# Kernel tuning notes

Hardware: AMD Instinct MI355X
Metric: run time of the kernel (lower is better)

Reference implementation:

```python
import jax, jax.numpy as jnp
import numpy as np
import math

N = 50000          # nodes
E = 1000000        # edges (avg degree 20)
NGRAPH = 64        # graphs in batch
CIN = 16           # input scalar channels (16x0e)
C = 32             # hidden multiplicity (mul)
OUT = 100          # output scalars per graph (100x0e)
NB = 10            # number_of_basis
MAX_RADIUS = 3.5
NUM_NEIGH = 20.0
NUM_NODES = 781.25 # 50000 / 64


def setup_inputs() -> dict:
    key = jax.random.key(0)
    ks = jax.random.split(key, 24)
    def p(k, shape, fan):
        return jax.random.normal(k, shape, jnp.float32) / math.sqrt(fan)
    inp = {}
    inp['pos'] = jax.random.normal(ks[0], (N, 3), jnp.float32)
    inp['x'] = jax.random.normal(ks[1], (N, CIN), jnp.float32)
    inp['z'] = jnp.ones((N, 1), jnp.float32)
    inp['edge_index'] = jax.random.randint(ks[2], (2, E), 0, N)
    inp['edge_shift'] = jnp.zeros((E, 3), jnp.float32)
    inp['lattice'] = jax.random.normal(ks[3], (NGRAPH, 3, 3), jnp.float32) * 0.01
    inp['batch'] = jnp.sort(jax.random.randint(ks[4], (N,), 0, NGRAPH))
    inp['fc1_w0'] = p(ks[5], (NB, 100), NB)
    inp['fc1_w1'] = p(ks[6], (100, 2 * CIN), 100)
    inp['sc1'] = p(ks[7], (CIN, 2 * C), CIN)
    inp['lin1_s'] = p(ks[8], (CIN, 2 * C), CIN)
    inp['lin1_v'] = p(ks[9], (CIN, C), CIN)
    inp['fc2_w0'] = p(ks[10], (NB, 100), NB)
    inp['fc2_w1'] = p(ks[11], (100, 5 * C), 100)
    inp['sc2_s'] = p(ks[12], (C, 2 * C), C)
    inp['sc2_v'] = p(ks[13], (C, C), C)
    inp['lin2_s'] = p(ks[14], (C, 2 * C), C)
    inp['lin2_v'] = p(ks[15], (C, C), C)
    inp['fco_w0'] = p(ks[16], (NB, 100), NB)
    inp['fco_w1'] = p(ks[17], (100, 2 * C), 100)
    inp['sco'] = p(ks[18], (C, OUT), C)
    inp['lino_s'] = p(ks[19], (C, OUT), C)
    return inp


def _edge_features(pos, edge_index, edge_shift, lattice, batch):
    src, dst = edge_index[0], edge_index[1]
    ebatch = batch[src]
    # preprocess: edge vectors with periodic shift correction
    edge_vec = pos[dst] - pos[src] + jnp.einsum('ni,nij->nj', edge_shift, lattice[ebatch])
    r = jnp.linalg.norm(edge_vec, axis=1)
    rhat = edge_vec / jnp.maximum(r, 1e-12)[:, None]
    # spherical harmonics lmax=1, component normalization: Y0 = 1, Y1 = sqrt(3) * rhat
    sh0 = jnp.ones_like(r)
    sh1 = math.sqrt(3.0) * rhat
    # soft_one_hot_linspace, basis='gaussian', cutoff=False, scaled by sqrt(NB)
    values = jnp.linspace(0.0, MAX_RADIUS, NB)
    step = values[1] - values[0]
    diff = (r[:, None] - values[None, :]) / step
    basis = jnp.exp(-diff * diff) / 1.12 * math.sqrt(NB)
    # smooth_cutoff(r / max_radius)
    u = 2.0 * (r / MAX_RADIUS - 1.0)
    cut = jnp.where(u > 0, 0.0, jnp.where(u < -2.0, 1.0, 0.5 * (1.0 - jnp.cos(math.pi * u))))
    return src, dst, cut * sh0, cut[:, None] * sh1, basis


def _seg(m, dst):
    return jax.ops.segment_sum(m, dst, num_segments=N) / math.sqrt(NUM_NEIGH)


def reference(pos, x, z, edge_index, edge_shift, lattice, batch,
              fc1_w0, fc1_w1, sc1, lin1_s, lin1_v,
              fc2_w0, fc2_w1, sc2_s, sc2_v, lin2_s, lin2_v,
              fco_w0, fco_w1, sco, lino_s):
    src, dst, sh0, sh1, basis = _edge_features(pos, edge_index, edge_shift, lattice, batch)

    # ---- layer 1: 16x0e input -> gated (C x 0e, C x 1o) ----
    w = jax.nn.silu(basis @ fc1_w0) @ fc1_w1           # (E, 2*CIN) radial weights
    s_src = x[src]                                     # (E, CIN)
    m_s = w[:, :CIN] * s_src * sh0[:, None]            # 0e x Y0 -> 0e
    m_v = (w[:, CIN:] * s_src)[:, :, None] * sh1[:, None, :]  # 0e x Y1 -> 1o
    a_s = _seg(m_s, dst)                               # (N, CIN)
    a_v = _seg(m_v, dst)                               # (N, CIN, 3)
    s_h = (x * z) @ sc1 + a_s @ lin1_s                 # (N, 2C) scalars+gates
    v_h = jnp.einsum('nci,co->noi', a_v, lin1_v)       # (N, C, 3)
    s = jax.nn.silu(s_h[:, :C])
    v = v_h * jax.nn.sigmoid(s_h[:, C:])[:, :, None]

    # ---- layer 2: (C x 0e, C x 1o) -> gated (C x 0e, C x 1o) ----
    w = jax.nn.silu(basis @ fc2_w0) @ fc2_w1           # (E, 5C)
    w1, w2, w3, w4, w5 = jnp.split(w, 5, axis=1)
    ss = s[src]                                        # (E, C)
    vs = v[src]                                        # (E, C, 3)
    m_s = w1 * ss * sh0[:, None] + w2 * jnp.einsum('eci,ei->ec', vs, sh1)
    m_v = (w3 * ss)[:, :, None] * sh1[:, None, :] \
        + w4[:, :, None] * vs * sh0[:, None, None] \
        + w5[:, :, None] * jnp.cross(vs, sh1[:, None, :])
    a_s = _seg(m_s, dst)
    a_v = _seg(m_v, dst)
    s_h = (s * z) @ sc2_s + a_s @ lin2_s
    v_h = jnp.einsum('nci,co->noi', v, sc2_v) + jnp.einsum('nci,co->noi', a_v, lin2_v)
    s2 = jax.nn.silu(s_h[:, :C])
    v2 = v_h * jax.nn.sigmoid(s_h[:, C:])[:, :, None]

    # ---- output convolution: -> 100x0e per node ----
    w = jax.nn.silu(basis @ fco_w0) @ fco_w1           # (E, 2C)
    w1, w2 = jnp.split(w, 2, axis=1)
    m = w1 * s2[src] * sh0[:, None] + w2 * jnp.einsum('eci,ei->ec', v2[src], sh1)
    a = _seg(m, dst)                                   # (N, C)
    out_nodes = (s2 * z) @ sco + a @ lino_s            # (N, OUT)

    # reduce_output: scatter over graphs, divide sqrt(num_nodes)
    out = jax.ops.segment_sum(out_nodes, batch, num_segments=NGRAPH) / math.sqrt(NUM_NODES)
    return out
```

## Files before the change

### kernel.cpp

```cpp
#include <hip/hip_runtime.h>
#include <hip/hip_bf16.h>

#define NN 50000
#define EE 1000000
#define NGRAPHS 64
#define NB_N 196
#define NB_E 3907
#define NB_X 3125
#define NB_T 1563
#define NTAB 4096
#define SPL 16

#define INV_SQRT_NEIGH 0.22360679774997896f
#define INV_SQRT_NODES 0.035777087639996634f
#define SQRT3 1.7320508075688772f
#define BSCALE 2.8234621879136734f
#define BSTEP 0.3888888888888889f
#define INV_BSTEP 2.5714285714285716f
#define PI_F 3.14159265358979323846f
#define TAB_DR (3.5f / 4095.0f)
#define TAB_SCALE (4095.0f / 3.5f)

__device__ __forceinline__ float silu_f(float x) { return x / (1.0f + __expf(-x)); }
__device__ __forceinline__ float sigm_f(float x) { return 1.0f / (1.0f + __expf(-x)); }

__device__ __forceinline__ unsigned short f2bf(float f) {
    union { float f; unsigned u; } v; v.f = f;
    unsigned r = v.u + 0x7fffu + ((v.u >> 16) & 1u);
    return (unsigned short)(r >> 16);
}
__device__ __forceinline__ unsigned pk2(float a, float b) {
    return (unsigned)f2bf(a) | ((unsigned)f2bf(b) << 16);
}
__device__ __forceinline__ float bflo(unsigned u) { return __uint_as_float(u << 16); }
__device__ __forceinline__ float bfhi(unsigned u) { return __uint_as_float(u & 0xffff0000u); }

__global__ __launch_bounds__(256) void k_tab(
    const float* __restrict__ fc1w0, const float* __restrict__ fc1w1,
    const float* __restrict__ fc2w0, const float* __restrict__ fc2w1,
    const float* __restrict__ fcow0, const float* __restrict__ fcow1,
    float* __restrict__ tab1, unsigned short* __restrict__ tab2b,
    unsigned short* __restrict__ tab3b)
{
    __shared__ float h[3][100];
    int entry = blockIdx.x;
    int t = threadIdx.x;
    float r = entry * TAB_DR;
    float b[10];
#pragma unroll
    for (int i = 0; i < 10; ++i) {
        float d = (r - (float)i * BSTEP) * INV_BSTEP;
        b[i] = __expf(-d * d) * BSCALE;
    }
    for (int job = t; job < 300; job += 256) {
        int tb = job / 100;
        int j = job - tb * 100;
        const float* w0 = (tb == 0) ? fc1w0 : (tb == 1 ? fc2w0 : fcow0);
        float a = 0.0f;
#pragma unroll
        for (int i = 0; i < 10; ++i) a += b[i] * w0[i * 100 + j];
        h[tb][j] = silu_f(a);
    }
    __syncthreads();
    if (t < 32) {
        float acc = 0.0f;
        for (int j = 0; j < 100; ++j) acc += h[0][j] * fc1w1[j * 32 + t];
        tab1[(size_t)entry * 32 + t] = acc;
    } else if (t < 192) {
        int o = t - 32;
        float acc = 0.0f;
        for (int j = 0; j < 100; ++j) acc += h[1][j] * fc2w1[j * 160 + o];
        tab2b[((size_t)entry * 32 + (o & 31)) * 8 + (o >> 5)] = f2bf(acc);
    } else {
        int o = t - 192;
        float acc = 0.0f;
        for (int j = 0; j < 100; ++j) acc += h[2][j] * fcow1[j * 64 + o];
        tab3b[((size_t)entry * 32 + (o & 31)) * 2 + (o >> 5)] = f2bf(acc);
    }
}

__global__ __launch_bounds__(256) void k_pre2(
    const int* __restrict__ batch, int* __restrict__ gstart,
    const int* __restrict__ ei, int* __restrict__ deg,
    const float* __restrict__ x, unsigned short* __restrict__ row0)
{
    int blk = blockIdx.x;
    if (blk < NB_N) {
        int n = blk * 256 + threadIdx.x;
        if (n >= NN) return;
        int b = batch[n];
        if (n == 0) { for (int g = 0; g <= b; ++g) gstart[g] = 0; }
        else {
            int pb = batch[n - 1];
            for (int g = pb + 1; g <= b; ++g) gstart[g] = n;
        }
        if (n == NN - 1) { for (int g = b + 1; g <= NGRAPHS; ++g) gstart[g] = NN; }
    } else if (blk < NB_N + NB_E) {
        int e = (blk - NB_N) * 256 + threadIdx.x;
        if (e < EE) atomicAdd(&deg[ei[EE + e]], 1);
    } else {
        int idx = (blk - NB_N - NB_E) * 256 + threadIdx.x;
        if (idx < NN * 16) row0[idx] = f2bf(x[idx]);
    }
}

__global__ __launch_bounds__(256) void k_scan1(const int* __restrict__ deg, int* __restrict__ bsum)
{
    __shared__ int sd[256];
    int t = threadIdx.x;
    int i = blockIdx.x * 256 + t;
    sd[t] = (i < NN) ? deg[i] : 0;
    __syncthreads();
#pragma unroll
    for (int o = 128; o > 0; o >>= 1) {
        if (t < o) sd[t] += sd[t + o];
        __syncthreads();
    }
    if (t == 0) bsum[blockIdx.x] = sd[0];
}

__global__ void k_scan2(const int* __restrict__ bsum, int* __restrict__ boff, int* __restrict__ rowp)
{
    if (threadIdx.x == 0) {
        int acc = 0;
        for (int b = 0; b < NB_N; ++b) { boff[b] = acc; acc += bsum[b]; }
        rowp[NN] = EE;
    }
}

__global__ __launch_bounds__(256) void k_scan3(
    const int* __restrict__ deg, const int* __restrict__ boff,
    int* __restrict__ rowp, int* __restrict__ cursor)
{
    __shared__ int sd[256];
    int t = threadIdx.x;
    int i = blockIdx.x * 256 + t;
    int v = (i < NN) ? deg[i] : 0;
    sd[t] = v;
    __syncthreads();
#pragma unroll
    for (int o = 1; o < 256; o <<= 1) {
        int xv = 0;
        if (t >= o) xv = sd[t - o];
        __syncthreads();
        sd[t] += xv;
        __syncthreads();
    }
    if (i < NN) {
        int val = boff[blockIdx.x] + sd[t] - v;
        rowp[i] = val;
        cursor[i] = val;
    }
}

__global__ __launch_bounds__(256) void k_geom(
    const float* __restrict__ pos, const int* __restrict__ ei,
    const float* __restrict__ eshift, const float* __restrict__ lat,
    const int* __restrict__ batch, int* __restrict__ cursor,
    uint4* __restrict__ rec)
{
    int e = blockIdx.x * 256 + threadIdx.x;
    if (e >= EE) return;
    int src = ei[e];
    int dst = ei[EE + e];
    int g = batch[src];
    const float* L = lat + g * 9;
    float t0 = eshift[e*3+0], t1 = eshift[e*3+1], t2 = eshift[e*3+2];
    float vx = pos[dst*3+0] - pos[src*3+0] + t0*L[0] + t1*L[3] + t2*L[6];
    float vy = pos[dst*3+1] - pos[src*3+1] + t0*L[1] + t1*L[4] + t2*L[7];
    float vz = pos[dst*3+2] - pos[src*3+2] + t0*L[2] + t1*L[5] + t2*L[8];
    float r = sqrtf(vx*vx + vy*vy + vz*vz);
    float u = 2.0f * (r * (1.0f/3.5f) - 1.0f);
    float cut;
    if (u > 0.0f) cut = 0.0f;
    else if (u < -2.0f) cut = 1.0f;
    else cut = 0.5f * (1.0f - __cosf(PI_F * u));
    float inv = 1.0f / fmaxf(r, 1e-12f);
    float sc = SQRT3 * cut * inv;
    int i0 = (int)fminf(r * TAB_SCALE + 0.5f, 4095.0f);
    int slot = atomicAdd(&cursor[dst], 1);
    rec[slot] = make_uint4(pk2(sc * vx, sc * vy), pk2(sc * vz, 0.0f),
                           (unsigned)src | ((unsigned)i0 << 17),
                           __float_as_uint(cut));
}

#define EREC_DECODE(E)                                  \
    float cs_ = __uint_as_float((E).w);                 \
    float cx_ = bflo((E).x);                            \
    float cy_ = bfhi((E).x);                            \
    float cz_ = bflo((E).y);                            \
    int src_ = (int)((E).z & 0x1ffffu);                 \
    int i0_ = (int)((E).z >> 17);

#define F1_EDGE(E, ACC) {                                           \
    EREC_DECODE(E)                                                  \
    float w_ = tab1[(size_t)i0_ * 32 + toff];                       \
    float xs_ = __uint_as_float((unsigned)row0[src_ * 16 + c] << 16); \
    float gs_ = (q == 0) ? cs_ : (q == 1 ? cx_ : (q == 2 ? cy_ : cz_)); \
    ACC += w_ * xs_ * gs_; }

__global__ __launch_bounds__(256) void k_fuse1(
    const int* __restrict__ rowp, const uint4* __restrict__ rec,
    const float* __restrict__ tab1, const unsigned short* __restrict__ row0,
    float* __restrict__ a1)
{
    int wid = (blockIdx.x * 256 + threadIdx.x) >> 6;
    int l = threadIdx.x & 63;
    if (wid >= NN) return;
    int b0 = __builtin_amdgcn_readfirstlane(rowp[wid]);
    int b1 = __builtin_amdgcn_readfirstlane(rowp[wid + 1]);
    int q = l >> 4, c = l & 15;
    int toff = (q ? 16 : 0) + c;
    float aA = 0.0f, aB = 0.0f, aC = 0.0f, aD = 0.0f;
    int s = b0;
    for (; s + 3 < b1; s += 4) {
        uint4 eA = rec[s], eB = rec[s+1], eC = rec[s+2], eD = rec[s+3];
        F1_EDGE(eA, aA) F1_EDGE(eB, aB) F1_EDGE(eC, aC) F1_EDGE(eD, aD)
    }
    for (; s < b1; ++s) {
        uint4 eA = rec[s];
        F1_EDGE(eA, aA)
    }
    a1[(size_t)wid * 64 + l] = (aA + aB) + (aC + aD);
}

#define F2_EDGE(E, AS, AX, AY, AZ) {                                \
    EREC_DECODE(E)                                                  \
    uint4 tv_ = ((const uint4*)tab2b)[(size_t)i0_ * 32 + c];        \
    uint2 rv_ = ((const uint2*)row1)[(size_t)src_ * 32 + c];        \
    float w1_ = bflo(tv_.x), w2_ = bfhi(tv_.x);                     \
    float w3_ = bflo(tv_.y), w4_ = bfhi(tv_.y);                     \
    float w5_ = bflo(tv_.z);                                        \
    float sv_ = bflo(rv_.x), vx_ = bfhi(rv_.x);                     \
    float vy_ = bflo(rv_.y), vz_ = bfhi(rv_.y);                     \
    float dot_ = vx_ * cx_ + vy_ * cy_ + vz_ * cz_;                 \
    float w3s_ = w3_ * sv_, w4c_ = w4_ * cs_;                       \
    AS += w1_ * sv_ * cs_ + w2_ * dot_;                             \
    AX += w3s_ * cx_ + w4c_ * vx_ + w5_ * (vy_ * cz_ - vz_ * cy_);  \
    AY += w3s_ * cy_ + w4c_ * vy_ + w5_ * (vz_ * cx_ - vx_ * cz_);  \
    AZ += w3s_ * cz_ + w4c_ * vz_ + w5_ * (vx_ * cy_ - vy_ * cx_); }

__global__ __launch_bounds__(256) void k_fuse2(
    const int* __restrict__ rowp, const uint4* __restrict__ rec,
    const unsigned short* __restrict__ tab2b, const unsigned short* __restrict__ row1,
    float* __restrict__ a2)
{
    int wid = (blockIdx.x * 256 + threadIdx.x) >> 6;
    int l = threadIdx.x & 63;
    if (wid >= NN) return;
    int b0 = __builtin_amdgcn_readfirstlane(rowp[wid]);
    int b1 = __builtin_amdgcn_readfirstlane(rowp[wid + 1]);
    int p = l >> 5, c = l & 31;
    float s0 = 0, x0 = 0, y0 = 0, z0 = 0;
    float s1a = 0, x1 = 0, y1 = 0, z1 = 0;
    int s = b0 + p;
    for (; s + 4 < b1; s += 6) {
        uint4 eA = rec[s], eB = rec[s+2], eC = rec[s+4];
        F2_EDGE(eA, s0, x0, y0, z0)
        F2_EDGE(eB, s1a, x1, y1, z1)
        F2_EDGE(eC, s0, x0, y0, z0)
    }
    for (; s < b1; s += 2) {
        uint4 eA = rec[s];
        F2_EDGE(eA, s1a, x1, y1, z1)
    }
    float mS = s0 + s1a, mX = x0 + x1, mY = y0 + y1, mZ = z0 + z1;
    mS += __shfl_xor(mS, 32);
    mX += __shfl_xor(mX, 32);
    mY += __shfl_xor(mY, 32);
    mZ += __shfl_xor(mZ, 32);
    if (p == 0) {
        float* ap = a2 + (size_t)wid * 128;
        ap[c]      = mS;
        ap[32 + c] = mX;
        ap[64 + c] = mY;
        ap[96 + c] = mZ;
    }
}

#define F3_EDGE(E, ACC) {                                           \
    EREC_DECODE(E)                                                  \
    unsigned tv_ = ((const unsigned*)tab3b)[(size_t)i0_ * 32 + c];  \
    uint2 rv_ = ((const uint2*)row2)[(size_t)src_ * 32 + c];        \
    float w1_ = bflo(tv_), w2_ = bfhi(tv_);                         \
    float sv_ = bflo(rv_.x), vx_ = bfhi(rv_.x);                     \
    float vy_ = bflo(rv_.y), vz_ = bfhi(rv_.y);                     \
    float dot_ = vx_ * cx_ + vy_ * cy_ + vz_ * cz_;                 \
    ACC += w1_ * sv_ * cs_ + w2_ * dot_; }

__global__ __launch_bounds__(256) void k_fuse3(
    const int* __restrict__ rowp, const uint4* __restrict__ rec,
    const unsigned short* __restrict__ tab3b, const unsigned short* __restrict__ row2,
    float* __restrict__ a3)
{
    int wid = (blockIdx.x * 256 + threadIdx.x) >> 6;
    int l = threadIdx.x & 63;
    if (wid >= NN) return;
    int b0 = __builtin_amdgcn_readfirstlane(rowp[wid]);
    int b1 = __builtin_amdgcn_readfirstlane(rowp[wid + 1]);
    int p = l >> 5, c = l & 31;
    float aA = 0.0f, aB = 0.0f;
    int s = b0 + p;
    for (; s + 6 < b1; s += 8) {
        uint4 eA = rec[s], eB = rec[s+2], eC = rec[s+4], eD = rec[s+6];
        F3_EDGE(eA, aA) F3_EDGE(eB, aB) F3_EDGE(eC, aA) F3_EDGE(eD, aB)
    }
    for (; s < b1; s += 2) {
        uint4 eA = rec[s];
        F3_EDGE(eA, aA)
    }
    float acc = aA + aB;
    acc += __shfl_xor(acc, 32);
    if (p == 0) a3[(size_t)wid * 32 + c] = acc;
}

__global__ __launch_bounds__(256) void k_node1(
    const float* __restrict__ x, const float* __restrict__ z,
    const float* __restrict__ a1,
    const float* __restrict__ sc1, const float* __restrict__ lin1s,
    const float* __restrict__ lin1v,
    ushort4* __restrict__ row1)
{
    __shared__ float xz[32][20];
    __shared__ float am[32][68];
    __shared__ float shb[32][68];
    int t = threadIdx.x;
    int base = blockIdx.x * 32;
    if (t < 128) {
        int node = t >> 2, rem = t & 3;
        if (base + node < NN)
            *(float4*)&xz[node][rem * 4] = ((const float4*)x)[(size_t)(base + node) * 4 + rem];
    }
#pragma unroll
    for (int k = 0; k < 2; ++k) {
        int f = k * 256 + t;
        int node = f >> 4, rem = f & 15;
        if (base + node < NN)
            *(float4*)&am[node][rem * 4] = ((const float4*)a1)[(size_t)(base + node) * 16 + rem];
    }
    __syncthreads();
    int node = t >> 3, og = t & 7;
    int gnode = base + node;
    float zz = (gnode < NN) ? z[gnode] : 0.0f;
    int o0 = og * 8;
    float acc[8];
#pragma unroll
    for (int k = 0; k < 8; ++k) acc[k] = 0.0f;
#pragma unroll
    for (int c = 0; c < 16; ++c) {
        float xc = xz[node][c] * zz;
        float ac = am[node][c] * INV_SQRT_NEIGH;
        float4 wa = *(const float4*)&sc1[c * 64 + o0];
        float4 wb = *(const float4*)&sc1[c * 64 + o0 + 4];
        float4 la = *(const float4*)&lin1s[c * 64 + o0];
        float4 lb = *(const float4*)&lin1s[c * 64 + o0 + 4];
        acc[0] += xc * wa.x + ac * la.x;
        acc[1] += xc * wa.y + ac * la.y;
        acc[2] += xc * wa.z + ac * la.z;
        acc[3] += xc * wa.w + ac * la.w;
        acc[4] += xc * wb.x + ac * lb.x;
        acc[5] += xc * wb.y + ac * lb.y;
        acc[6] += xc * wb.z + ac * lb.z;
        acc[7] += xc * wb.w + ac * lb.w;
    }
#pragma unroll
    for (int k = 0; k < 8; ++k) shb[node][o0 + k] = acc[k];
    __syncthreads();
    int o0v = og * 4;
    float a4[3][4];
#pragma unroll
    for (int i = 0; i < 3; ++i)
#pragma unroll
        for (int k = 0; k < 4; ++k) a4[i][k] = 0.0f;
#pragma unroll
    for (int c = 0; c < 16; ++c) {
        float4 lv = *(const float4*)&lin1v[c * 32 + o0v];
#pragma unroll
        for (int i = 0; i < 3; ++i) {
            float av = am[node][16 + i * 16 + c] * INV_SQRT_NEIGH;
            a4[i][0] += av * lv.x; a4[i][1] += av * lv.y;
            a4[i][2] += av * lv.z; a4[i][3] += av * lv.w;
        }
    }
    if (gnode < NN) {
#pragma unroll
        for (int k = 0; k < 4; ++k) {
            float so = silu_f(shb[node][o0v + k]);
            float gt = sigm_f(shb[node][32 + o0v + k]);
            row1[(size_t)gnode * 32 + o0v + k] =
                make_ushort4(f2bf(so), f2bf(a4[0][k] * gt), f2bf(a4[1][k] * gt), f2bf(a4[2][k] * gt));
        }
    }
}

__global__ __launch_bounds__(256) void k_node2(
    const float* __restrict__ z,
    const uint2* __restrict__ row1, const float* __restrict__ a2,
    const float* __restrict__ sc2s, const float* __restrict__ sc2v,
    const float* __restrict__ lin2s, const float* __restrict__ lin2v,
    float* __restrict__ s2, ushort4* __restrict__ row2)
{
    __shared__ uint2 rw[32][33];
    __shared__ float am[32][132];
    __shared__ float shb[32][68];
    int t = threadIdx.x;
    int base = blockIdx.x * 32;
    {
        int node = t >> 3, rem = t & 7;
        if (base + node < NN) {
            const uint2* rp = row1 + (size_t)(base + node) * 32;
#pragma unroll
            for (int k = 0; k < 4; ++k)
                rw[node][rem * 4 + k] = rp[rem * 4 + k];
        }
    }
#pragma unroll
    for (int k = 0; k < 4; ++k) {
        int f = k * 256 + t;
        int node = f >> 5, rem = f & 31;
        if (base + node < NN)
            *(float4*)&am[node][rem * 4] = ((const float4*)a2)[(size_t)(base + node) * 32 + rem];
    }
    __syncthreads();
    int node = t >> 3, og = t & 7;
    int gnode = base + node;
    float zz = (gnode < NN) ? z[gnode] : 0.0f;
    int o0 = og * 8;
    float acc[8];
#pragma unroll
    for (int k = 0; k < 8; ++k) acc[k] = 0.0f;
#pragma unroll 8
    for (int c = 0; c < 32; ++c) {
        float sv = bflo(rw[node][c].x) * zz;
        float ac = am[node][c] * INV_SQRT_NEIGH;
        float4 wa = *(const float4*)&sc2s[c * 64 + o0];
        float4 wb = *(const float4*)&sc2s[c * 64 + o0 + 4];
        float4 la = *(const float4*)&lin2s[c * 64 + o0];
        float4 lb = *(const float4*)&lin2s[c * 64 + o0 + 4];
        acc[0] += sv * wa.x + ac * la.x;
        acc[1] += sv * wa.y + ac * la.y;
        acc[2] += sv * wa.z + ac * la.z;
        acc[3] += sv * wa.w + ac * la.w;
        acc[4] += sv * wb.x + ac * lb.x;
        acc[5] += sv * wb.y + ac * lb.y;
        acc[6] += sv * wb.z + ac * lb.z;
        acc[7] += sv * wb.w + ac * lb.w;
    }
#pragma unroll
    for (int k = 0; k < 8; ++k) shb[node][o0 + k] = acc[k];
    __syncthreads();
    int o0v = og * 4;
    float a4[3][4];
#pragma unroll
    for (int i = 0; i < 3; ++i)
#pragma unroll
        for (int k = 0; k < 4; ++k) a4[i][k] = 0.0f;
#pragma unroll 8
    for (int c = 0; c < 32; ++c) {
        float4 wv = *(const float4*)&sc2v[c * 32 + o0v];
        float4 lv = *(const float4*)&lin2v[c * 32 + o0v];
        uint2 rv = rw[node][c];
        float vvv[3];
        vvv[0] = bfhi(rv.x); vvv[1] = bflo(rv.y); vvv[2] = bfhi(rv.y);
#pragma unroll
        for (int i = 0; i < 3; ++i) {
            float av = am[node][32 + i * 32 + c] * INV_SQRT_NEIGH;
            a4[i][0] += vvv[i] * wv.x + av * lv.x;
            a4[i][1] += vvv[i] * wv.y + av * lv.y;
            a4[i][2] += vvv[i] * wv.z + av * lv.z;
            a4[i][3] += vvv[i] * wv.w + av * lv.w;
        }
    }
    if (gnode < NN) {
#pragma unroll
        for (int k = 0; k < 4; ++k) {
            float so = silu_f(shb[node][o0v + k]);
            float gt = sigm_f(shb[node][32 + o0v + k]);
            s2[gnode * 32 + o0v + k] = so;
            row2[(size_t)gnode * 32 + o0v + k] =
                make_ushort4(f2bf(so), f2bf(a4[0][k] * gt), f2bf(a4[1][k] * gt), f2bf(a4[2][k] * gt));
        }
    }
}

__global__ __launch_bounds__(256) void k_red(
    const float* __restrict__ z, const int* __restrict__ gstart,
    const float* __restrict__ s2, const float* __restrict__ a3,
    float* __restrict__ pbuf)
{
    int g  = blockIdx.x >> 4;
    int sp = blockIdx.x & (SPL - 1);
    int n0 = gstart[g], n1 = gstart[g + 1];
    int per = (n1 - n0 + SPL - 1) / SPL;
    int a = n0 + sp * per;
    int b = a + per; if (b > n1) b = n1;
    int t = threadIdx.x;
    int comp = t & 63;
    int lane = t >> 6;
    float acc = 0.0f;
    for (int n = a + lane; n < b; n += 4) {
        if (comp < 32) acc += s2[n * 32 + comp] * z[n];
        else           acc += a3[(size_t)n * 32 + (comp - 32)];
    }
    __shared__ float sd[256];
    sd[t] = acc;
    __syncthreads();
    if (t < 64)
        pbuf[(size_t)blockIdx.x * 64 + t] = sd[t] + sd[t + 64] + sd[t + 128] + sd[t + 192];
}

__global__ __launch_bounds__(128) void k_out2(
    const float* __restrict__ pbuf, const float* __restrict__ sco,
    const float* __restrict__ lino, float* __restrict__ out)
{
    __shared__ float A[32], B[32];
    int g = blockIdx.x;
    int t = threadIdx.x;
    if (t < 64) {
        float v = 0.0f;
        for (int sp = 0; sp < SPL; ++sp)
            v += pbuf[(size_t)(g * SPL + sp) * 64 + t];
        if (t < 32) A[t] = v;
        else        B[t - 32] = v * INV_SQRT_NEIGH;
    }
    __syncthreads();
    if (t < 100) {
        float res = 0.0f;
#pragma unroll
        for (int c = 0; c < 32; ++c)
            res += A[c] * sco[c * 100 + t] + B[c] * lino[c * 100 + t];
        out[g * 100 + t] = res * INV_SQRT_NODES;
    }
}

extern "C" void kernel_launch(void* const* d_in, const int* in_sizes, int n_in,
                              void* d_out, int out_size, void* d_ws, size_t ws_size,
                              hipStream_t stream)
{
    const float* pos   = (const float*)d_in[0];
    const float* x     = (const float*)d_in[1];
    const float* z     = (const float*)d_in[2];
    const int*   ei    = (const int*)d_in[3];
    const float* esh   = (const float*)d_in[4];
    const float* lat   = (const float*)d_in[5];
    const int*   batch = (const int*)d_in[6];
    const float* fc1w0 = (const float*)d_in[7];
    const float* fc1w1 = (const float*)d_in[8];
    const float* sc1   = (const float*)d_in[9];
    const float* lin1s = (const float*)d_in[10];
    const float* lin1v = (const float*)d_in[11];
    const float* fc2w0 = (const float*)d_in[12];
    const float* fc2w1 = (const float*)d_in[13];
    const float* sc2s  = (const float*)d_in[14];
    const float* sc2v  = (const float*)d_in[15];
    const float* lin2s = (const float*)d_in[16];
    const float* lin2v = (const float*)d_in[17];
    const float* fcow0 = (const float*)d_in[18];
    const float* fcow1 = (const float*)d_in[19];
    const float* sco   = (const float*)d_in[20];
    const float* lino  = (const float*)d_in[21];
    float* out = (float*)d_out;

    char* cur = (char*)d_ws;
    auto alloc = [&](size_t bytes) { char* r = cur; cur += (bytes + 15) & ~(size_t)15; return r; };

    float* a1    = (float*)alloc((size_t)NN * 64 * 4);
    float* a2    = (float*)alloc((size_t)NN * 128 * 4);
    float* a3    = (float*)alloc((size_t)NN * 32 * 4);
    float* s2    = (float*)alloc((size_t)NN * 32 * 4);
    unsigned short* row0 = (unsigned short*)alloc((size_t)NN * 16 * 2);
    ushort4* row1 = (ushort4*)alloc((size_t)NN * 32 * 8);
    ushort4* row2 = (ushort4*)alloc((size_t)NN * 32 * 8);
    float* tab1  = (float*)alloc((size_t)NTAB * 32 * 4);
    unsigned short* tab2b = (unsigned short*)alloc((size_t)NTAB * 32 * 8 * 2);
    unsigned short* tab3b = (unsigned short*)alloc((size_t)NTAB * 32 * 2 * 2);
    float* pbuf  = (float*)alloc((size_t)NGRAPHS * SPL * 64 * 4);
    int* deg     = (int*)alloc((size_t)NN * 4);
    int* rowp    = (int*)alloc((size_t)(NN + 4) * 4);
    int* cursor  = (int*)alloc((size_t)NN * 4);
    int* bsum    = (int*)alloc(256 * 4);
    int* boff    = (int*)alloc(256 * 4);
    int* gstart  = (int*)alloc(68 * 4);
    uint4* rec   = (uint4*)alloc((size_t)EE * 16);

    (void)hipMemsetAsync(deg, 0, (size_t)NN * 4, stream);

    k_tab<<<NTAB, 256, 0, stream>>>(fc1w0, fc1w1, fc2w0, fc2w1, fcow0, fcow1,
                                    tab1, tab2b, tab3b);
    k_pre2<<<NB_N + NB_E + NB_X, 256, 0, stream>>>(batch, gstart, ei, deg, x, row0);

    k_scan1<<<NB_N, 256, 0, stream>>>(deg, bsum);
    k_scan2<<<1, 64, 0, stream>>>(bsum, boff, rowp);
    k_scan3<<<NB_N, 256, 0, stream>>>(deg, boff, rowp, cursor);
    k_geom <<<NB_E, 256, 0, stream>>>(pos, ei, esh, lat, batch, cursor, rec);

    int fb = (NN * 64 + 255) / 256;
    k_fuse1<<<fb, 256, 0, stream>>>(rowp, rec, tab1, row0, a1);
    k_node1<<<NB_T, 256, 0, stream>>>(x, z, a1, sc1, lin1s, lin1v, row1);
    k_fuse2<<<fb, 256, 0, stream>>>(rowp, rec, tab2b, (const unsigned short*)row1, a2);
    k_node2<<<NB_T, 256, 0, stream>>>(z, (const uint2*)row1, a2, sc2s, sc2v, lin2s, lin2v, s2, row2);
    k_fuse3<<<fb, 256, 0, stream>>>(rowp, rec, tab3b, (const unsigned short*)row2, a3);
    k_red<<<NGRAPHS * SPL, 256, 0, stream>>>(z, gstart, s2, a3, pbuf);
    k_out2<<<NGRAPHS, 128, 0, stream>>>(pbuf, sco, lino, out);
}
```

Measured before the change: 368.6 us.

## Merge table and preprocessing kernels, store conv2 table as fp32, unroll fuse2

Folds the radial-table kernel into the preprocessing kernel so a single launch covers table build, graph starts, degree counting and bf16 conversion. The conv2 weight table is now stored in fp32 rather than bf16, removing the unpacking work and bf16 rounding at the cost of twice the table footprint (4 MB). The fuse2 edge loop is unrolled from three to four edges per step. The table is indexed by the gathered edge radius, so the wider fp32 entries may put more pressure on the cache.

```diff
diff --git a/kernel.cpp b/kernel.cpp
--- a/kernel.cpp
+++ b/kernel.cpp
@@ -35,58 +35,55 @@
 __device__ __forceinline__ float bflo(unsigned u) { return __uint_as_float(u << 16); }
 __device__ __forceinline__ float bfhi(unsigned u) { return __uint_as_float(u & 0xffff0000u); }
 
-__global__ __launch_bounds__(256) void k_tab(
+__global__ __launch_bounds__(256) void k_pre3(
     const float* __restrict__ fc1w0, const float* __restrict__ fc1w1,
     const float* __restrict__ fc2w0, const float* __restrict__ fc2w1,
     const float* __restrict__ fcow0, const float* __restrict__ fcow1,
-    float* __restrict__ tab1, unsigned short* __restrict__ tab2b,
-    unsigned short* __restrict__ tab3b)
-{
-    __shared__ float h[3][100];
-    int entry = blockIdx.x;
-    int t = threadIdx.x;
-    float r = entry * TAB_DR;
-    float b[10];
-#pragma unroll
-    for (int i = 0; i < 10; ++i) {
-        float d = (r - (float)i * BSTEP) * INV_BSTEP;
-        b[i] = __expf(-d * d) * BSCALE;
-    }
-    for (int job = t; job < 300; job += 256) {
-        int tb = job / 100;
-        int j = job - tb * 100;
-        const float* w0 = (tb == 0) ? fc1w0 : (tb == 1 ? fc2w0 : fcow0);
-        float a = 0.0f;
-#pragma unroll
-        for (int i = 0; i < 10; ++i) a += b[i] * w0[i * 100 + j];
-        h[tb][j] = silu_f(a);
-    }
-    __syncthreads();
-    if (t < 32) {
-        float acc = 0.0f;
-        for (int j = 0; j < 100; ++j) acc += h[0][j] * fc1w1[j * 32 + t];
-        tab1[(size_t)entry * 32 + t] = acc;
-    } else if (t < 192) {
-        int o = t - 32;
-        float acc = 0.0f;
-        for (int j = 0; j < 100; ++j) acc += h[1][j] * fc2w1[j * 160 + o];
-        tab2b[((size_t)entry * 32 + (o & 31)) * 8 + (o >> 5)] = f2bf(acc);
-    } else {
-        int o = t - 192;
-        float acc = 0.0f;
-        for (int j = 0; j < 100; ++j) acc += h[2][j] * fcow1[j * 64 + o];
-        tab3b[((size_t)entry * 32 + (o & 31)) * 2 + (o >> 5)] = f2bf(acc);
-    }
-}
-
-__global__ __launch_bounds__(256) void k_pre2(
+    float* __restrict__ tab1, float* __restrict__ tab2f,
+    unsigned short* __restrict__ tab3b,
     const int* __restrict__ batch, int* __restrict__ gstart,
     const int* __restrict__ ei, int* __restrict__ deg,
     const float* __restrict__ x, unsigned short* __restrict__ row0)
 {
     int blk = blockIdx.x;
-    if (blk < NB_N) {
-        int n = blk * 256 + threadIdx.x;
+    int t = threadIdx.x;
+    if (blk < NTAB) {
+        __shared__ float h[3][100];
+        int entry = blk;
+        float r = entry * TAB_DR;
+        float b[10];
+#pragma unroll
+        for (int i = 0; i < 10; ++i) {
+            float d = (r - (float)i * BSTEP) * INV_BSTEP;
+            b[i] = __expf(-d * d) * BSCALE;
+        }
+        for (int job = t; job < 300; job += 256) {
+            int tb = job / 100;
+            int j = job - tb * 100;
+            const float* w0 = (tb == 0) ? fc1w0 : (tb == 1 ? fc2w0 : fcow0);
+            float a = 0.0f;
+#pragma unroll
+            for (int i = 0; i < 10; ++i) a += b[i] * w0[i * 100 + j];
+            h[tb][j] = silu_f(a);
+        }
+        __syncthreads();
+        if (t < 32) {
+            float acc = 0.0f;
+            for (int j = 0; j < 100; ++j) acc += h[0][j] * fc1w1[j * 32 + t];
+            tab1[(size_t)entry * 32 + t] = acc;
+        } else if (t < 192) {
+            int o = t - 32;
+            float acc = 0.0f;
+            for (int j = 0; j < 100; ++j) acc += h[1][j] * fc2w1[j * 160 + o];
+            tab2f[((size_t)entry * 32 + (o & 31)) * 8 + (o >> 5)] = acc;
+        } else {
+            int o = t - 192;
+            float acc = 0.0f;
+            for (int j = 0; j < 100; ++j) acc += h[2][j] * fcow1[j * 64 + o];
+            tab3b[((size_t)entry * 32 + (o & 31)) * 2 + (o >> 5)] = f2bf(acc);
+        }
+    } else if (blk < NTAB + NB_N) {
+        int n = (blk - NTAB) * 256 + t;
         if (n >= NN) return;
         int b = batch[n];
         if (n == 0) { for (int g = 0; g <= b; ++g) gstart[g] = 0; }
@@ -95,11 +92,11 @@
             for (int g = pb + 1; g <= b; ++g) gstart[g] = n;
         }
         if (n == NN - 1) { for (int g = b + 1; g <= NGRAPHS; ++g) gstart[g] = NN; }
-    } else if (blk < NB_N + NB_E) {
-        int e = (blk - NB_N) * 256 + threadIdx.x;
+    } else if (blk < NTAB + NB_N + NB_E) {
+        int e = (blk - NTAB - NB_N) * 256 + t;
         if (e < EE) atomicAdd(&deg[ei[EE + e]], 1);
     } else {
-        int idx = (blk - NB_N - NB_E) * 256 + threadIdx.x;
+        int idx = (blk - NTAB - NB_N - NB_E) * 256 + t;
         if (idx < NN * 16) row0[idx] = f2bf(x[idx]);
     }
 }
@@ -226,23 +223,22 @@
 
 #define F2_EDGE(E, AS, AX, AY, AZ) {                                \
     EREC_DECODE(E)                                                  \
-    uint4 tv_ = ((const uint4*)tab2b)[(size_t)i0_ * 32 + c];        \
+    const float* tp_ = tab2f + ((size_t)i0_ * 32 + c) * 8;          \
+    float4 w14_ = *(const float4*)tp_;                              \
+    float w5_ = tp_[4];                                             \
     uint2 rv_ = ((const uint2*)row1)[(size_t)src_ * 32 + c];        \
-    float w1_ = bflo(tv_.x), w2_ = bfhi(tv_.x);                     \
-    float w3_ = bflo(tv_.y), w4_ = bfhi(tv_.y);                     \
-    float w5_ = bflo(tv_.z);                                        \
     float sv_ = bflo(rv_.x), vx_ = bfhi(rv_.x);                     \
     float vy_ = bflo(rv_.y), vz_ = bfhi(rv_.y);                     \
     float dot_ = vx_ * cx_ + vy_ * cy_ + vz_ * cz_;                 \
-    float w3s_ = w3_ * sv_, w4c_ = w4_ * cs_;                       \
-    AS += w1_ * sv_ * cs_ + w2_ * dot_;                             \
+    float w3s_ = w14_.z * sv_, w4c_ = w14_.w * cs_;                 \
+    AS += w14_.x * sv_ * cs_ + w14_.y * dot_;                       \
     AX += w3s_ * cx_ + w4c_ * vx_ + w5_ * (vy_ * cz_ - vz_ * cy_);  \
     AY += w3s_ * cy_ + w4c_ * vy_ + w5_ * (vz_ * cx_ - vx_ * cz_);  \
     AZ += w3s_ * cz_ + w4c_ * vz_ + w5_ * (vx_ * cy_ - vy_ * cx_); }
 
 __global__ __launch_bounds__(256) void k_fuse2(
     const int* __restrict__ rowp, const uint4* __restrict__ rec,
-    const unsigned short* __restrict__ tab2b, const unsigned short* __restrict__ row1,
+    const float* __restrict__ tab2f, const unsigned short* __restrict__ row1,
     float* __restrict__ a2)
 {
     int wid = (blockIdx.x * 256 + threadIdx.x) >> 6;
@@ -254,11 +250,12 @@
     float s0 = 0, x0 = 0, y0 = 0, z0 = 0;
     float s1a = 0, x1 = 0, y1 = 0, z1 = 0;
     int s = b0 + p;
-    for (; s + 4 < b1; s += 6) {
-        uint4 eA = rec[s], eB = rec[s+2], eC = rec[s+4];
+    for (; s + 6 < b1; s += 8) {
+        uint4 eA = rec[s], eB = rec[s+2], eC = rec[s+4], eD = rec[s+6];
         F2_EDGE(eA, s0, x0, y0, z0)
         F2_EDGE(eB, s1a, x1, y1, z1)
         F2_EDGE(eC, s0, x0, y0, z0)
+        F2_EDGE(eD, s1a, x1, y1, z1)
     }
     for (; s < b1; s += 2) {
         uint4 eA = rec[s];
@@ -572,7 +569,7 @@
     ushort4* row1 = (ushort4*)alloc((size_t)NN * 32 * 8);
     ushort4* row2 = (ushort4*)alloc((size_t)NN * 32 * 8);
     float* tab1  = (float*)alloc((size_t)NTAB * 32 * 4);
-    unsigned short* tab2b = (unsigned short*)alloc((size_t)NTAB * 32 * 8 * 2);
+    float* tab2f = (float*)alloc((size_t)NTAB * 32 * 8 * 4);
     unsigned short* tab3b = (unsigned short*)alloc((size_t)NTAB * 32 * 2 * 2);
     float* pbuf  = (float*)alloc((size_t)NGRAPHS * SPL * 64 * 4);
     int* deg     = (int*)alloc((size_t)NN * 4);
@@ -585,9 +582,9 @@
 
     (void)hipMemsetAsync(deg, 0, (size_t)NN * 4, stream);
 
-    k_tab<<<NTAB, 256, 0, stream>>>(fc1w0, fc1w1, fc2w0, fc2w1, fcow0, fcow1,
-                                    tab1, tab2b, tab3b);
-    k_pre2<<<NB_N + NB_E + NB_X, 256, 0, stream>>>(batch, gstart, ei, deg, x, row0);
+    k_pre3<<<NTAB + NB_N + NB_E + NB_X, 256, 0, stream>>>(
+        fc1w0, fc1w1, fc2w0, fc2w1, fcow0, fcow1, tab1, tab2f, tab3b,
+        batch, gstart, ei, deg, x, row0);
 
     k_scan1<<<NB_N, 256, 0, stream>>>(deg, bsum);
     k_scan2<<<1, 64, 0, stream>>>(bsum, boff, rowp);
@@ -597,7 +594,7 @@
     int fb = (NN * 64 + 255) / 256;
     k_fuse1<<<fb, 256, 0, stream>>>(rowp, rec, tab1, row0, a1);
     k_node1<<<NB_T, 256, 0, stream>>>(x, z, a1, sc1, lin1s, lin1v, row1);
-    k_fuse2<<<fb, 256, 0, stream>>>(rowp, rec, tab2b, (const unsigned short*)row1, a2);
+    k_fuse2<<<fb, 256, 0, stream>>>(rowp, rec, tab2f, (const unsigned short*)row1, a2);
     k_node2<<<NB_T, 256, 0, stream>>>(z, (const uint2*)row1, a2, sc2s, sc2v, lin2s, lin2v, s2, row2);
     k_fuse3<<<fb, 256, 0, stream>>>(rowp, rec, tab3b, (const unsigned short*)row2, a3);
     k_red<<<NGRAPHS * SPL, 256, 0, stream>>>(z, gstart, s2, a3, pbuf);
```

New measurement: 412.0 us. 1.12x slower.
